# Performance work log

Measured on AMD Instinct MI355X. Metric: run time of the kernel, lower is better.

## Reference

```python
import jax, jax.numpy as jnp
import numpy as np

# --- model dims (ModelArgs defaults) ---
DIM = 1024      # model dim
NH = 12         # n_heads
NOPE = 128      # qk_nope_head_dim
ROPE = 64       # qk_rope_head_dim (32 complex pairs)
QKH = NOPE + ROPE  # 192
VH = 128        # v_head_dim
KVR = 512       # kv_lora_rank
B, S = 4, 2048
EPS = 1e-6
SM_SCALE = QKH ** -0.5  # max_seq_len <= original_seq_len -> no mscale


def setup_inputs() -> dict:
    key = jax.random.key(0)
    ks = jax.random.split(key, 6)
    std = lambda fan_in: 0.02 / np.sqrt(fan_in)
    x = jax.random.normal(ks[0], (B, S, DIM), jnp.float32)
    wq = jax.random.normal(ks[1], (NH * QKH, DIM), jnp.float32) * std(DIM)
    wkv_a = jax.random.normal(ks[2], (KVR + ROPE, DIM), jnp.float32) * std(DIM)
    kv_norm_w = jnp.ones((KVR,), jnp.float32)
    wkv_b = jax.random.normal(ks[3], (NH * (NOPE + VH), KVR), jnp.float32) * std(KVR)
    wo = jax.random.normal(ks[4], (DIM, NH * VH), jnp.float32) * std(NH * VH)
    # rotary freqs_cis for positions [0, S): cos/sin of pos * theta^(-2i/ROPE)
    inv_freq = 1.0 / (10000.0 ** (np.arange(0, ROPE, 2, dtype=np.float32) / ROPE))
    ang = np.outer(np.arange(S, dtype=np.float32), inv_freq)  # [S, 32]
    freqs_cis = jnp.stack([jnp.cos(ang), jnp.sin(ang)], axis=-1).astype(jnp.float32)  # [S,32,2]
    # causal mask [S, S]: -inf above diagonal
    i = jnp.arange(S)
    mask = jnp.where(i[None, :] > i[:, None], -jnp.inf, 0.0).astype(jnp.float32)
    return {"x": x, "wq": wq, "wkv_a": wkv_a, "kv_norm_w": kv_norm_w,
            "wkv_b": wkv_b, "wo": wo, "freqs_cis": freqs_cis, "mask": mask,
            "start_pos": 0}


def rmsnorm(x, w, eps=EPS):
    xf = x.astype(jnp.float32)
    return (xf * jax.lax.rsqrt(jnp.mean(xf * xf, axis=-1, keepdims=True) + eps) * w).astype(x.dtype)


def apply_rope(x, freqs_cis):
    # x: [B, S, H, D]; pairs are consecutive last-dim elements (view_as_complex semantics)
    x2 = x.reshape(*x.shape[:-1], -1, 2)
    xr, xi = x2[..., 0], x2[..., 1]
    fr = freqs_cis[..., 0][None, :, None, :]  # [1, S, 1, D/2]
    fi = freqs_cis[..., 1][None, :, None, :]
    yr = xr * fr - xi * fi
    yi = xr * fi + xi * fr
    return jnp.stack([yr, yi], axis=-1).reshape(x.shape).astype(x.dtype)


def reference(x, wq, wkv_a, kv_norm_w, wkv_b, wo, freqs_cis, mask, start_pos):
    bsz, seqlen, _ = x.shape
    # q projection (q_lora_rank == 0 path)
    q = (x @ wq.T).reshape(bsz, seqlen, NH, QKH)
    q_nope, q_pe = q[..., :NOPE], q[..., NOPE:]
    q_pe = apply_rope(q_pe, freqs_cis)
    # low-rank kv projection
    kv_full = x @ wkv_a.T                       # [B,S,KVR+ROPE]
    kv, k_pe = kv_full[..., :KVR], kv_full[..., KVR:]
    k_pe = apply_rope(k_pe[:, :, None, :], freqs_cis)[:, :, 0, :]  # [B,S,ROPE]
    # absorb k-side of wkv_b into q (MLA absorption)
    wkv_b3 = wkv_b.reshape(NH, NOPE + VH, KVR)
    q_nope = jnp.einsum('bshd,hdc->bshc', q_nope, wkv_b3[:, :NOPE])  # [B,S,H,KVR]
    # latent caches (detached in original module)
    kv_c = jax.lax.stop_gradient(rmsnorm(kv, kv_norm_w))  # [B,S,KVR]
    pe_c = jax.lax.stop_gradient(k_pe)                    # [B,S,ROPE]
    scores = (jnp.einsum('bshc,btc->bsht', q_nope, kv_c)
              + jnp.einsum('bshr,btr->bsht', q_pe, pe_c)) * SM_SCALE
    scores = scores + mask[None, :, None, :]
    attn = jax.nn.softmax(scores.astype(jnp.float32), axis=-1).astype(x.dtype)
    o = jnp.einsum('bsht,btc->bshc', attn, kv_c)           # [B,S,H,KVR]
    o = jnp.einsum('bshc,hdc->bshd', o, wkv_b3[:, NOPE:])  # [B,S,H,VH]
    return o.reshape(bsz, seqlen, NH * VH) @ wo.T           # [B,S,DIM]
```

## Files before the change

### kernel.cpp

```cpp
#include <hip/hip_runtime.h>

typedef __bf16 bf16;
typedef __bf16 bf16x8 __attribute__((ext_vector_type(8)));
typedef __bf16 bf16x4 __attribute__((ext_vector_type(4)));
typedef float floatx4 __attribute__((ext_vector_type(4)));

#define T_TOK 8192
#define SEQ 2048
#define KLD 584
#define SM_SCALE 0.07216878364870323f
#define NJOBS 768

__device__ __forceinline__ void dma16(const void* g, void* l) {
  __builtin_amdgcn_global_load_lds(
      (const __attribute__((address_space(1))) unsigned int*)g,
      (__attribute__((address_space(3))) unsigned int*)l, 16, 0, 0);
}

__device__ __forceinline__ void sync_vm() {
  __builtin_amdgcn_sched_barrier(0);
  asm volatile("s_waitcnt vmcnt(0) lgkmcnt(0)");
  __builtin_amdgcn_s_barrier();
  __builtin_amdgcn_sched_barrier(0);
}
__device__ __forceinline__ void sync_lg() {
  __builtin_amdgcn_sched_barrier(0);
  asm volatile("s_waitcnt lgkmcnt(0)");
  __builtin_amdgcn_s_barrier();
  __builtin_amdgcn_sched_barrier(0);
}

__global__ __launch_bounds__(256) void cast_f32_bf16(const float* __restrict__ in,
                                                     bf16* __restrict__ out, long n4) {
  long i = (long)blockIdx.x * 256 + threadIdx.x;
  if (i >= n4) return;
  float4 v = ((const float4*)in)[i];
  bf16x4 o;
  o[0] = (bf16)v.x; o[1] = (bf16)v.y; o[2] = (bf16)v.z; o[3] = (bf16)v.w;
  ((bf16x4*)out)[i] = o;
}

__global__ __launch_bounds__(256) void cast_wkva_pad(const float* __restrict__ in,
                                                     bf16* __restrict__ out) {
  long i = (long)blockIdx.x * 256 + threadIdx.x;
  int r = (int)(i >> 8);
  bf16x4 o;
  if (r < 576) {
    float4 v = ((const float4*)in)[i];
    o[0] = (bf16)v.x; o[1] = (bf16)v.y; o[2] = (bf16)v.z; o[3] = (bf16)v.w;
  } else {
    o[0] = (bf16)0.f; o[1] = (bf16)0.f; o[2] = (bf16)0.f; o[3] = (bf16)0.f;
  }
  ((bf16x4*)out)[i] = o;
}

__global__ __launch_bounds__(256) void split_wkvb(const float* __restrict__ in,
                                                  bf16* __restrict__ wbnT,
                                                  bf16* __restrict__ wbv,
                                                  int* __restrict__ ctr) {
  if (blockIdx.x == 0 && threadIdx.x == 0) *ctr = 0;
  int i = blockIdx.x * 256 + threadIdx.x;
  int h = i >> 17, rem = i & 131071, d = rem >> 9, c = rem & 511;
  bf16 v = (bf16)in[i];
  if (d < 128) wbnT[((h * 512 + c) << 7) + d] = v;
  else         wbv[((h * 128 + (d - 128)) << 9) + c] = v;
}

template <int MODE>
__global__ __launch_bounds__(256) void gemm_bt(
    const bf16* __restrict__ A, const bf16* __restrict__ B, void* __restrict__ Cv,
    int N, int K, int lda, int ldb, int ldc,
    long sA, long sB, long sC,
    const float* __restrict__ freqs, bf16* __restrict__ qn, bf16* __restrict__ qabs) {
  __shared__ alignas(16) bf16 As[128 * 32];
  __shared__ alignas(16) bf16 Bs[128 * 32];
  const int z = blockIdx.z;
  A += (long)z * sA;  B += (long)z * sB;
  const int row0 = blockIdx.y * 128, col0 = blockIdx.x * 128;
  const int tid = threadIdx.x;
  const int w = tid >> 6, l = tid & 63, lm = l & 15, quad = l >> 4;
  const int wr = w >> 1, wc = w & 1;
  floatx4 acc[4][4] = {};

  const int srow = l >> 2, scol = (l & 3) * 8;

  for (int k0 = 0; k0 < K; k0 += 32) {
    __syncthreads();
#pragma unroll
    for (int c = 0; c < 2; c++) {
      const int ch = w * 2 + c;
      dma16(A + (long)(row0 + 16 * ch + srow) * lda + k0 + scol, (char*)As + ch * 1024);
      dma16(B + (long)(col0 + 16 * ch + srow) * ldb + k0 + scol, (char*)Bs + ch * 1024);
    }
    __syncthreads();
    bf16x8 af[4], bfr[4];
#pragma unroll
    for (int i = 0; i < 4; i++) {
      af[i]  = *(const bf16x8*)(As + (wr * 64 + i * 16 + lm) * 32 + quad * 8);
      bfr[i] = *(const bf16x8*)(Bs + (wc * 64 + i * 16 + lm) * 32 + quad * 8);
    }
#pragma unroll
    for (int i = 0; i < 4; i++)
#pragma unroll
      for (int j = 0; j < 4; j++)
        acc[i][j] = __builtin_amdgcn_mfma_f32_16x16x32_bf16(af[i], bfr[j], acc[i][j], 0, 0, 0);
  }

  if constexpr (MODE == 3) {
    __shared__ alignas(16) bf16 Ts[128 * 136];
#pragma unroll
    for (int i = 0; i < 4; i++)
#pragma unroll
      for (int j = 0; j < 4; j++)
#pragma unroll
        for (int r = 0; r < 4; r++) {
          const int tl = wr * 64 + i * 16 + quad * 4 + r;
          const int cl = wc * 64 + j * 16 + lm;
          Ts[cl * 136 + tl] = (bf16)acc[i][j][r];
        }
    __syncthreads();
    bf16* Cb = (bf16*)Cv + (long)z * sC;
    const int t4 = (l & 31) * 4;
#pragma unroll
    for (int pp = 0; pp < 16; pp++) {
      const int d = pp * 8 + w * 2 + (l >> 5);
      *(uint2*)(Cb + (long)d * ldc + row0 + t4) = *(const uint2*)(Ts + d * 136 + t4);
    }
  } else {
#pragma unroll
    for (int i = 0; i < 4; i++) {
#pragma unroll
      for (int j = 0; j < 4; j++) {
#pragma unroll
        for (int r = 0; r < 4; r++) {
          float val = acc[i][j][r];
          float partner = __shfl_xor(val, 1, 64);
          int rr = row0 + wr * 64 + i * 16 + quad * 4 + r;
          int cc = col0 + wc * 64 + j * 16 + lm;
          if (cc < N) {
            if (MODE == 0) {
              ((float*)Cv + (long)z * sC)[(long)rr * ldc + cc] = val;
            } else if (MODE == 1) {
              ((bf16*)Cv + (long)z * sC)[(long)rr * ldc + cc] = (bf16)val;
            } else {
              int s = rr & (SEQ - 1);
              int h = cc / 192, wi = cc % 192;
              if (wi < 128) {
                qn[((long)h * T_TOK + rr) * 128 + wi] = (bf16)(val * SM_SCALE);
              } else {
                int pp = (wi - 128) >> 1;
                float cs = freqs[s * 64 + pp * 2], sn = freqs[s * 64 + pp * 2 + 1];
                float res = ((wi & 1) == 0) ? (val * cs - partner * sn)
                                            : (partner * sn + val * cs);
                qabs[((long)h * T_TOK + rr) * 576 + 512 + (wi - 128)] = (bf16)(res * SM_SCALE);
              }
            }
          }
        }
      }
    }
  }
}

__global__ __launch_bounds__(64) void kvnorm_rope(const float* __restrict__ kvf,
                                                  const float* __restrict__ wnorm,
                                                  const float* __restrict__ freqs,
                                                  bf16* __restrict__ Kp) {
  const int t = blockIdx.x, l = threadIdx.x, s = t & (SEQ - 1);
  const float* row = kvf + (long)t * 576;
  float4 a4 = ((const float4*)row)[l * 2];
  float4 b4 = ((const float4*)row)[l * 2 + 1];
  float v[8] = {a4.x, a4.y, a4.z, a4.w, b4.x, b4.y, b4.z, b4.w};
  float ssq = 0.f;
#pragma unroll
  for (int i = 0; i < 8; i++) ssq += v[i] * v[i];
#pragma unroll
  for (int m = 1; m < 64; m <<= 1) ssq += __shfl_xor(ssq, m, 64);
  const float rn = rsqrtf(ssq * (1.f / 512.f) + 1e-6f);
  bf16x8 o;
#pragma unroll
  for (int i = 0; i < 8; i++) o[i] = (bf16)(v[i] * rn * wnorm[l * 8 + i]);
  *(bf16x8*)(Kp + (long)t * KLD + l * 8) = o;
  if (l < 32) {
    float xr = row[512 + 2 * l], xi = row[513 + 2 * l];
    float cs = freqs[s * 64 + 2 * l], sn = freqs[s * 64 + 2 * l + 1];
    Kp[(long)t * KLD + 512 + 2 * l] = (bf16)(xr * cs - xi * sn);
    Kp[(long)t * KLD + 513 + 2 * l] = (bf16)(xr * sn + xi * cs);
  }
}

__global__ __attribute__((amdgpu_waves_per_eu(2, 2))) __launch_bounds__(512)
void mla_attn(const bf16* __restrict__ qabs,
              const bf16* __restrict__ Kp,
              const bf16* __restrict__ VpT,
              bf16* __restrict__ o_all,
              int* __restrict__ ctr) {
  constexpr int PROW = 36;
  __shared__ alignas(16) bf16 Ks[2][20480];
  __shared__ alignas(16) bf16 Ps[4 * 32 * PROW];
  __shared__ float alpha_s[128];
  __shared__ float l_s[128];
  __shared__ int jid_s;

  const int tid = threadIdx.x, w = tid >> 6, l = tid & 63;
  const int lm = l & 15, quad = l >> 4;
  const bool isS = (w < 4);
  const int h4 = w & 3;

  for (;;) {
    __syncthreads();
    if (tid == 0) jid_s = atomicAdd(ctr, 1);
    __syncthreads();
    const int j = jid_s;
    if (j >= NJOBS) return;

    const int mac = 63 - j / 12;
    const int bg = j % 12;
    const int b = bg & 3, g = bg >> 2;
    const int nk = mac + 1;
    const long tq0 = (long)b * SEQ + mac * 32;
    const bf16* KpB = Kp + (long)b * SEQ * KLD;

    if (isS) {
      bf16x8 qf[2][18];
#pragma unroll
      for (int n = 0; n < 2; n++) {
        const bf16* qb =
            qabs + ((long)(g * 4 + h4) * T_TOK + tq0 + n * 16 + lm) * 576 + quad * 8;
#pragma unroll
        for (int kk = 0; kk < 18; kk++) qf[n][kk] = *(const bf16x8*)(qb + kk * 32);
      }
      float mstate[2] = {-__builtin_inff(), -__builtin_inff()};
      float lstate[2] = {0.f, 0.f};

      for (int kt = 0; kt < nk; kt++) {
        sync_vm();
        const bf16* Kcur = Ks[kt & 1];

        floatx4 sacc[2][2] = {};
#pragma unroll
        for (int kk = 0; kk < 18; kk++) {
          bf16x8 kf0 = *(const bf16x8*)(Kcur + lm * KLD + kk * 32 + quad * 8);
          bf16x8 kf1 = *(const bf16x8*)(Kcur + (16 + lm) * KLD + kk * 32 + quad * 8);
          sacc[0][0] = __builtin_amdgcn_mfma_f32_16x16x32_bf16(kf0, qf[0][kk], sacc[0][0], 0, 0, 0);
          sacc[0][1] = __builtin_amdgcn_mfma_f32_16x16x32_bf16(kf0, qf[1][kk], sacc[0][1], 0, 0, 0);
          sacc[1][0] = __builtin_amdgcn_mfma_f32_16x16x32_bf16(kf1, qf[0][kk], sacc[1][0], 0, 0, 0);
          sacc[1][1] = __builtin_amdgcn_mfma_f32_16x16x32_bf16(kf1, qf[1][kk], sacc[1][1], 0, 0, 0);
        }
        if (kt == nk - 1) {
#pragma unroll
          for (int m = 0; m < 2; m++)
#pragma unroll
            for (int n = 0; n < 2; n++)
#pragma unroll
              for (int r = 0; r < 4; r++)
                if (m * 16 + quad * 4 + r > n * 16 + lm) sacc[m][n][r] = -__builtin_inff();
        }
#pragma unroll
        for (int n = 0; n < 2; n++) {
          float cmax = -__builtin_inff();
#pragma unroll
          for (int m = 0; m < 2; m++)
#pragma unroll
            for (int r = 0; r < 4; r++) cmax = fmaxf(cmax, sacc[m][n][r]);
          cmax = fmaxf(cmax, __shfl_xor(cmax, 16, 64));
          cmax = fmaxf(cmax, __shfl_xor(cmax, 32, 64));
          const float mnew = fmaxf(mstate[n], cmax);
          const float alpha = __expf(mstate[n] - mnew);
          float psum = 0.f;
#pragma unroll
          for (int m = 0; m < 2; m++) {
            bf16x4 pw;
#pragma unroll
            for (int r = 0; r < 4; r++) {
              float pv = __expf(sacc[m][n][r] - mnew);
              psum += pv;
              pw[r] = (bf16)pv;
            }
            *(bf16x4*)(Ps + (h4 * 32 + n * 16 + lm) * PROW + m * 16 + quad * 4) = pw;
          }
          psum += __shfl_xor(psum, 16, 64);
          psum += __shfl_xor(psum, 32, 64);
          lstate[n] = lstate[n] * alpha + psum;
          mstate[n] = mnew;
          if (quad == 0) alpha_s[h4 * 32 + n * 16 + lm] = alpha;
        }
        sync_lg();
      }
      if (quad == 0) {
        l_s[h4 * 32 + lm] = lstate[0];
        l_s[h4 * 32 + 16 + lm] = lstate[1];
      }
      __syncthreads();
    } else {
      floatx4 oacc[2][8] = {};

      {
#pragma unroll
        for (int jj = 0; jj < 10; jj++)
          dma16((const char*)KpB + (h4 + jj * 4) * 1024 + l * 16,
                (char*)Ks[0] + (h4 + jj * 4) * 1024);
      }

      for (int kt = 0; kt < nk; kt++) {
        sync_vm();
        bf16x8 vb[8];
        const long tv = (long)b * SEQ + kt * 32 + quad * 8;
#pragma unroll
        for (int dt = 0; dt < 8; dt++) {
          const bf16* vrow =
              VpT + ((long)((g * 4 + h4) * 128 + dt * 16 + lm)) * T_TOK + tv;
          vb[dt] = *(const bf16x8*)(vrow);
        }
        {
          const int ktn = (kt + 1 < nk) ? kt + 1 : kt;
          const char* gk = (const char*)(KpB + (long)ktn * 32 * KLD);
          char* ld = (char*)Ks[(kt + 1) & 1];
#pragma unroll
          for (int jj = 0; jj < 10; jj++)
            dma16(gk + (h4 + jj * 4) * 1024 + l * 16, ld + (h4 + jj * 4) * 1024);
        }
        sync_lg();

#pragma unroll
        for (int qt = 0; qt < 2; qt++) {
#pragma unroll
          for (int r = 0; r < 4; r++) {
            const float a = alpha_s[h4 * 32 + qt * 16 + quad * 4 + r];
#pragma unroll
            for (int dt = 0; dt < 8; dt++) oacc[qt][dt][r] *= a;
          }
          bf16x8 pa = *(const bf16x8*)(Ps + (h4 * 32 + qt * 16 + lm) * PROW + quad * 8);
#pragma unroll
          for (int dt = 0; dt < 8; dt++)
            oacc[qt][dt] =
                __builtin_amdgcn_mfma_f32_16x16x32_bf16(pa, vb[dt], oacc[qt][dt], 0, 0, 0);
        }
      }
      __syncthreads();

#pragma unroll
      for (int qt = 0; qt < 2; qt++) {
#pragma unroll
        for (int r = 0; r < 4; r++) {
          const int qrow = qt * 16 + quad * 4 + r;
          const float inv = 1.f / l_s[h4 * 32 + qrow];
#pragma unroll
          for (int dt = 0; dt < 8; dt++)
            o_all[(tq0 + qrow) * 1536 + (g * 4 + h4) * 128 + dt * 16 + lm] =
                (bf16)(oacc[qt][dt][r] * inv);
        }
      }
    }
  }
}

extern "C" void kernel_launch(void* const* d_in, const int* in_sizes, int n_in,
                              void* d_out, int out_size, void* d_ws, size_t ws_size,
                              hipStream_t stream) {
  (void)in_sizes; (void)n_in; (void)out_size; (void)ws_size;
  const float* x     = (const float*)d_in[0];
  const float* wq    = (const float*)d_in[1];
  const float* wkva  = (const float*)d_in[2];
  const float* kvnw  = (const float*)d_in[3];
  const float* wkvb  = (const float*)d_in[4];
  const float* wo    = (const float*)d_in[5];
  const float* freqs = (const float*)d_in[6];
  float* out = (float*)d_out;

  char* p = (char*)d_ws;
  auto alloc = [&](size_t bytes) {
    char* r = p;
    p += (bytes + 255) & ~(size_t)255;
    return r;
  };
  bf16*  xb    = (bf16*) alloc((size_t)T_TOK * 1024 * 2);
  bf16*  wqb   = (bf16*) alloc((size_t)2304 * 1024 * 2);
  bf16*  wkvab = (bf16*) alloc((size_t)640 * 1024 * 2);
  bf16*  wbnT  = (bf16*) alloc((size_t)12 * 512 * 128 * 2);
  bf16*  wbv   = (bf16*) alloc((size_t)12 * 128 * 512 * 2);
  bf16*  wob   = (bf16*) alloc((size_t)1024 * 1536 * 2);
  float* kvf   = (float*)alloc((size_t)T_TOK * 576 * 4);
  bf16*  Kp    = (bf16*) alloc((size_t)T_TOK * KLD * 2 + 4096);
  bf16*  VpT   = (bf16*) alloc((size_t)12 * 128 * T_TOK * 2);
  bf16*  qn    = (bf16*) alloc((size_t)12 * T_TOK * 128 * 2);
  bf16*  qabs  = (bf16*) alloc((size_t)12 * T_TOK * 576 * 2);
  bf16*  o_all = (bf16*) alloc((size_t)T_TOK * 1536 * 2);
  int*   ctr   = (int*)  alloc(256);

  cast_f32_bf16<<<8192, 256, 0, stream>>>(x, xb, (long)T_TOK * 1024 / 4);
  cast_f32_bf16<<<2304, 256, 0, stream>>>(wq, wqb, (long)2304 * 1024 / 4);
  cast_wkva_pad<<<640, 256, 0, stream>>>(wkva, wkvab);
  split_wkvb<<<6144, 256, 0, stream>>>(wkvb, wbnT, wbv, ctr);
  cast_f32_bf16<<<1536, 256, 0, stream>>>(wo, wob, (long)1024 * 1536 / 4);

  gemm_bt<0><<<dim3(5, 64, 1), 256, 0, stream>>>(xb, wkvab, (void*)kvf, 576, 1024,
      1024, 1024, 576, 0, 0, 0, nullptr, nullptr, nullptr);
  gemm_bt<2><<<dim3(18, 64, 1), 256, 0, stream>>>(xb, wqb, nullptr, 2304, 1024,
      1024, 1024, 0, 0, 0, 0, freqs, qn, qabs);
  kvnorm_rope<<<T_TOK, 64, 0, stream>>>(kvf, kvnw, freqs, Kp);
  gemm_bt<3><<<dim3(1, 64, 12), 256, 0, stream>>>(Kp, wbv, (void*)VpT, 128, 512,
      KLD, 512, T_TOK, 0, (long)128 * 512, (long)128 * T_TOK,
      nullptr, nullptr, nullptr);
  gemm_bt<1><<<dim3(4, 64, 12), 256, 0, stream>>>(qn, wbnT, (void*)qabs, 512, 128,
      128, 128, 576, (long)T_TOK * 128, (long)512 * 128, (long)T_TOK * 576,
      nullptr, nullptr, nullptr);
  mla_attn<<<dim3(256, 1, 1), 512, 0, stream>>>(qabs, Kp, VpT, o_all, ctr);
  gemm_bt<0><<<dim3(8, 64, 1), 256, 0, stream>>>(o_all, wob, (void*)out, 1024, 1536,
      1536, 1536, 1024, 0, 0, 0, nullptr, nullptr, nullptr);
}
```

Baseline: 583.7 us.

## Software-pipeline score and PV waves with double-buffered P and one barrier

Double-buffers the probability tile and the alpha rescale factors so the PV waves work on tile kt-1 while the score waves compute tile kt. The two barriers per iteration become a single barrier. This removes the serialization where the PV waves idled waiting for softmax output and the score waves waited for PV consumption. In exchange it adds shared memory for the second P/alpha buffer and a skewed loop with an epilogue, and the DMA completion wait is now merged into the single full barrier.

Result: no change. 579.9 us (-0.6%).

```diff
diff --git a/kernel.cpp b/kernel.cpp
--- a/kernel.cpp
+++ b/kernel.cpp
@@ -17,15 +17,9 @@
       (__attribute__((address_space(3))) unsigned int*)l, 16, 0, 0);
 }
 
-__device__ __forceinline__ void sync_vm() {
+__device__ __forceinline__ void sync_all() {
   __builtin_amdgcn_sched_barrier(0);
   asm volatile("s_waitcnt vmcnt(0) lgkmcnt(0)");
-  __builtin_amdgcn_s_barrier();
-  __builtin_amdgcn_sched_barrier(0);
-}
-__device__ __forceinline__ void sync_lg() {
-  __builtin_amdgcn_sched_barrier(0);
-  asm volatile("s_waitcnt lgkmcnt(0)");
   __builtin_amdgcn_s_barrier();
   __builtin_amdgcn_sched_barrier(0);
 }
@@ -197,8 +191,8 @@
               int* __restrict__ ctr) {
   constexpr int PROW = 36;
   __shared__ alignas(16) bf16 Ks[2][20480];
-  __shared__ alignas(16) bf16 Ps[4 * 32 * PROW];
-  __shared__ float alpha_s[128];
+  __shared__ alignas(16) bf16 Ps[2][4 * 32 * PROW];
+  __shared__ float alpha_s[2][128];
   __shared__ float l_s[128];
   __shared__ int jid_s;
 
@@ -233,9 +227,12 @@
       float mstate[2] = {-__builtin_inff(), -__builtin_inff()};
       float lstate[2] = {0.f, 0.f};
 
+      sync_all();
+
       for (int kt = 0; kt < nk; kt++) {
-        sync_vm();
         const bf16* Kcur = Ks[kt & 1];
+        bf16* Pcur = Ps[kt & 1];
+        float* Acur = alpha_s[kt & 1];
 
         floatx4 sacc[2][2] = {};
 #pragma unroll
@@ -277,15 +274,15 @@
               psum += pv;
               pw[r] = (bf16)pv;
             }
-            *(bf16x4*)(Ps + (h4 * 32 + n * 16 + lm) * PROW + m * 16 + quad * 4) = pw;
+            *(bf16x4*)(Pcur + (h4 * 32 + n * 16 + lm) * PROW + m * 16 + quad * 4) = pw;
           }
           psum += __shfl_xor(psum, 16, 64);
           psum += __shfl_xor(psum, 32, 64);
           lstate[n] = lstate[n] * alpha + psum;
           mstate[n] = mnew;
-          if (quad == 0) alpha_s[h4 * 32 + n * 16 + lm] = alpha;
-        }
-        sync_lg();
+          if (quad == 0) Acur[h4 * 32 + n * 16 + lm] = alpha;
+        }
+        sync_all();
       }
       if (quad == 0) {
         l_s[h4 * 32 + lm] = lstate[0];
@@ -301,36 +298,68 @@
           dma16((const char*)KpB + (h4 + jj * 4) * 1024 + l * 16,
                 (char*)Ks[0] + (h4 + jj * 4) * 1024);
       }
+      sync_all();
 
       for (int kt = 0; kt < nk; kt++) {
-        sync_vm();
         bf16x8 vb[8];
-        const long tv = (long)b * SEQ + kt * 32 + quad * 8;
+        if (kt > 0) {
+          const long tv = (long)b * SEQ + (kt - 1) * 32 + quad * 8;
+#pragma unroll
+          for (int dt = 0; dt < 8; dt++) {
+            const bf16* vrow =
+                VpT + ((long)((g * 4 + h4) * 128 + dt * 16 + lm)) * T_TOK + tv;
+            vb[dt] = *(const bf16x8*)(vrow);
+          }
+        }
+        {
+          const int ktn = (kt + 1 < nk) ? kt + 1 : kt;
+          const char* gk = (const char*)(KpB + (long)ktn * 32 * KLD);
+          char* ld = (char*)Ks[(kt + 1) & 1];
+#pragma unroll
+          for (int jj = 0; jj < 10; jj++)
+            dma16(gk + (h4 + jj * 4) * 1024 + l * 16, ld + (h4 + jj * 4) * 1024);
+        }
+        if (kt > 0) {
+          const bf16* Pprev = Ps[(kt - 1) & 1];
+          const float* Aprev = alpha_s[(kt - 1) & 1];
+#pragma unroll
+          for (int qt = 0; qt < 2; qt++) {
+#pragma unroll
+            for (int r = 0; r < 4; r++) {
+              const float a = Aprev[h4 * 32 + qt * 16 + quad * 4 + r];
+#pragma unroll
+              for (int dt = 0; dt < 8; dt++) oacc[qt][dt][r] *= a;
+            }
+            bf16x8 pa = *(const bf16x8*)(Pprev + (h4 * 32 + qt * 16 + lm) * PROW + quad * 8);
+#pragma unroll
+            for (int dt = 0; dt < 8; dt++)
+              oacc[qt][dt] =
+                  __builtin_amdgcn_mfma_f32_16x16x32_bf16(pa, vb[dt], oacc[qt][dt], 0, 0, 0);
+          }
+        }
+        sync_all();
+      }
+
+      {
+        bf16x8 vb[8];
+        const long tv = (long)b * SEQ + (nk - 1) * 32 + quad * 8;
 #pragma unroll
         for (int dt = 0; dt < 8; dt++) {
           const bf16* vrow =
               VpT + ((long)((g * 4 + h4) * 128 + dt * 16 + lm)) * T_TOK + tv;
           vb[dt] = *(const bf16x8*)(vrow);
         }
-        {
-          const int ktn = (kt + 1 < nk) ? kt + 1 : kt;
-          const char* gk = (const char*)(KpB + (long)ktn * 32 * KLD);
-          char* ld = (char*)Ks[(kt + 1) & 1];
-#pragma unroll
-          for (int jj = 0; jj < 10; jj++)
-            dma16(gk + (h4 + jj * 4) * 1024 + l * 16, ld + (h4 + jj * 4) * 1024);
-        }
-        sync_lg();
-
+        const bf16* Pprev = Ps[(nk - 1) & 1];
+        const float* Aprev = alpha_s[(nk - 1) & 1];
 #pragma unroll
         for (int qt = 0; qt < 2; qt++) {
 #pragma unroll
           for (int r = 0; r < 4; r++) {
-            const float a = alpha_s[h4 * 32 + qt * 16 + quad * 4 + r];
+            const float a = Aprev[h4 * 32 + qt * 16 + quad * 4 + r];
 #pragma unroll
             for (int dt = 0; dt < 8; dt++) oacc[qt][dt][r] *= a;
           }
-          bf16x8 pa = *(const bf16x8*)(Ps + (h4 * 32 + qt * 16 + lm) * PROW + quad * 8);
+          bf16x8 pa = *(const bf16x8*)(Pprev + (h4 * 32 + qt * 16 + lm) * PROW + quad * 8);
 #pragma unroll
           for (int dt = 0; dt < 8; dt++)
             oacc[qt][dt] =
```
